# Kernel optimization log

Measured on AMD Instinct MI355X. Metric: run time of the kernel, lower is better.

## Reference

```python
import jax, jax.numpy as jnp
import numpy as np

_EPS = 1e-8
TEMPERATURE = 0.1  # head_cfg.temperature
WEIGHT = 1.0       # float(head_cfg.weight[1:]) with weight='w1'
N = 100000
K = 31   # nsample - 1
C = 64
NUM_CLASSES = 17


def setup_inputs() -> dict:
    key = jax.random.key(0)
    k1, k2, k3 = jax.random.split(key, 3)
    features = jax.random.normal(k1, (N, C), dtype=jnp.float32)
    labels = jax.random.randint(k2, (N,), 0, NUM_CLASSES, dtype=jnp.int32)
    # KNN neighbor indices with self excluded (original drops idx[...,1:]);
    # offset trick guarantees neighbor_idx[i, j] != i.
    off = jax.random.randint(k3, (N, K), 1, N, dtype=jnp.int32)
    neighbor_idx = (jnp.arange(N, dtype=jnp.int32)[:, None] + off) % N
    return {"features": features, "labels": labels, "neighbor_idx": neighbor_idx}


def reference(features, labels, neighbor_idx):
    # posmask_cnt: argmax of one-hot labels == integer class-id comparison
    neighbor_label = labels[neighbor_idx]                      # (N, K) int
    posmask = labels[:, None] == neighbor_label                # (N, K) bool
    cnt = posmask.sum(axis=1)
    point_mask = (cnt > 0) & (cnt < K)                          # (N,) bool

    # dist_l2 on gathered neighbor features
    neighbor_feature = features[neighbor_idx]                  # (N, K, C)
    diff = features[:, None, :] - neighbor_feature             # (N, K, C)
    dist = jnp.sqrt(jnp.sum(diff * diff, axis=-1)) + _EPS      # (N, K)

    # contrast_softnn
    logits = -dist
    logits = logits - jnp.max(logits, axis=1, keepdims=True)
    logits = logits / TEMPERATURE
    exp = jnp.exp(logits)                                      # (N, K)
    pos = jnp.sum(exp * posmask, axis=1)
    neg = jnp.sum(exp, axis=1)
    loss = -jnp.log(pos / neg + _EPS)                          # (N,)

    # masked mean == torch.mean(loss[point_mask])
    pm = point_mask.astype(loss.dtype)
    denom = jnp.maximum(jnp.sum(pm), 1.0)
    return jnp.sum(loss * pm) / denom * WEIGHT
```

## Files before the change

kernel.cpp:

```cpp
#include <hip/hip_runtime.h>
#include <hip/hip_fp16.h>

#define KNB 31
#define CH 64
#define TEMP_INV 10.0f

typedef _Float16 h2 __attribute__((ext_vector_type(2)));
typedef float f2 __attribute__((ext_vector_type(2)));


__global__ void ch_init_ws(double* __restrict__ ws, unsigned* __restrict__ ctr) {
    ws[0] = 0.0;
    ws[1] = 0.0;
    *ctr  = 0u;
}

__global__ __launch_bounds__(256) void ch_cvt8(
    const float* __restrict__ in, unsigned char* __restrict__ out,
    double* __restrict__ ws, unsigned* __restrict__ ctr, int total8)
{
    const int idx = blockIdx.x * blockDim.x + threadIdx.x;
    if (idx == 0) { ws[0] = 0.0; ws[1] = 0.0; *ctr = 0u; }
    if (idx >= total8) return;
    const float4* ip = reinterpret_cast<const float4*>(in) + (size_t)idx * 2;
    const float4 a = ip[0];
    const float4 b = ip[1];
    unsigned lo = 0u, hi = 0u;
    lo = __builtin_amdgcn_cvt_pk_fp8_f32(a.x, a.y, lo, false);
    lo = __builtin_amdgcn_cvt_pk_fp8_f32(a.z, a.w, lo, true);
    hi = __builtin_amdgcn_cvt_pk_fp8_f32(b.x, b.y, hi, false);
    hi = __builtin_amdgcn_cvt_pk_fp8_f32(b.z, b.w, hi, true);
    uint2 o; o.x = lo; o.y = hi;
    reinterpret_cast<uint2*>(out)[idx] = o;
}

__device__ __forceinline__ void fp8_to_f32x16(const uint4 u, float* f) {
    union { uint4 v; unsigned w[4]; } U;
    U.v = u;
    #pragma unroll
    for (int q = 0; q < 4; ++q) {
        const f2 p0 = __builtin_amdgcn_cvt_pk_f32_fp8(U.w[q], false);
        const f2 p1 = __builtin_amdgcn_cvt_pk_f32_fp8(U.w[q], true);
        f[4 * q + 0] = p0[0]; f[4 * q + 1] = p0[1];
        f[4 * q + 2] = p1[0]; f[4 * q + 3] = p1[1];
    }
}

__device__ __forceinline__ float fp8_sub_sq_acc(const float* fA, const uint4 bu, float s) {
    union { uint4 v; unsigned w[4]; } U;
    U.v = bu;
    #pragma unroll
    for (int q = 0; q < 4; ++q) {
        const f2 p0 = __builtin_amdgcn_cvt_pk_f32_fp8(U.w[q], false);
        const f2 p1 = __builtin_amdgcn_cvt_pk_f32_fp8(U.w[q], true);
        float d;
        d = fA[4 * q + 0] - p0[0]; s = fmaf(d, d, s);
        d = fA[4 * q + 1] - p0[1]; s = fmaf(d, d, s);
        d = fA[4 * q + 2] - p1[0]; s = fmaf(d, d, s);
        d = fA[4 * q + 3] - p1[1]; s = fmaf(d, d, s);
    }
    return s;
}

__global__ __launch_bounds__(256)
__attribute__((amdgpu_waves_per_eu(2, 4)))
void ch_main8q2(
    const unsigned char* __restrict__ tab8,
    const int*           __restrict__ labels,
    const int*           __restrict__ nidx,
    double*              __restrict__ ws,
    unsigned*            __restrict__ ctr,
    float*               __restrict__ out,
    int n)
{
    const int t    = threadIdx.x;
    const int qid  = t >> 2;
    const int sub  = t & 3;
    const int i0   = blockIdx.x * 128 + qid;
    const int i1   = i0 + 64;
    const bool v0  = (i0 < n);
    const bool v1  = (i1 < n);
    const int i0c  = v0 ? i0 : 0;
    const int i1c  = v1 ? i1 : 0;

    float loss_w = 0.0f;
    float pm_f   = 0.0f;

    if (v0) {
        float fA0[16], fA1[16];
        fp8_to_f32x16(reinterpret_cast<const uint4*>(tab8 + (size_t)i0c * CH)[sub], fA0);
        fp8_to_f32x16(reinterpret_cast<const uint4*>(tab8 + (size_t)i1c * CH)[sub], fA1);

        const int lab0 = labels[i0c];
        const int lab1 = labels[i1c];
        const int* nrow0 = nidx + (size_t)i0c * KNB;
        const int* nrow1 = nidx + (size_t)i1c * KNB;

        float m0 = -1e30f, se0 = 0.0f, sp0 = 0.0f;
        float m1 = -1e30f, se1 = 0.0f, sp1 = 0.0f;
        int cnt0 = 0, cnt1 = 0;

        #pragma unroll 2
        for (int j = 0; j < KNB; ++j) {
            const int nj0 = nrow0[j];
            const int nj1 = nrow1[j];

            const uint4 b0 = reinterpret_cast<const uint4*>(tab8 + (size_t)nj0 * CH)[sub];
            const uint4 b1 = reinterpret_cast<const uint4*>(tab8 + (size_t)nj1 * CH)[sub];

            float s0 = fp8_sub_sq_acc(fA0, b0, 0.0f);
            float s1 = fp8_sub_sq_acc(fA1, b1, 0.0f);

            s0 += __shfl_xor(s0, 1);
            s0 += __shfl_xor(s0, 2);
            s1 += __shfl_xor(s1, 1);
            s1 += __shfl_xor(s1, 2);

            const float l0 = -(sqrtf(s0) + 1e-8f);
            const float l1 = -(sqrtf(s1) + 1e-8f);

            const bool pm0 = (labels[nj0] == lab0);
            const bool pm1 = (labels[nj1] == lab1);
            cnt0 += pm0 ? 1 : 0;
            cnt1 += pm1 ? 1 : 0;

            if (l0 > m0) {
                const float r = __expf((m0 - l0) * TEMP_INV);
                se0 *= r; sp0 *= r; m0 = l0;
            }
            const float e0 = __expf((l0 - m0) * TEMP_INV);
            se0 += e0;
            if (pm0) sp0 += e0;

            if (l1 > m1) {
                const float r = __expf((m1 - l1) * TEMP_INV);
                se1 *= r; sp1 *= r; m1 = l1;
            }
            const float e1 = __expf((l1 - m1) * TEMP_INV);
            se1 += e1;
            if (pm1) sp1 += e1;
        }

        if (sub == 0) {
            if (v0 && cnt0 > 0 && cnt0 < KNB) {
                loss_w += -logf(sp0 / se0 + 1e-8f);
                pm_f   += 1.0f;
            }
            if (v1 && cnt1 > 0 && cnt1 < KNB) {
                loss_w += -logf(sp1 / se1 + 1e-8f);
                pm_f   += 1.0f;
            }
        }
    }

    __shared__ float s_l[256];
    __shared__ float s_c[256];
    s_l[t] = loss_w;
    s_c[t] = pm_f;
    __syncthreads();
    #pragma unroll
    for (int off = 128; off > 0; off >>= 1) {
        if (t < off) {
            s_l[t] += s_l[t + off];
            s_c[t] += s_c[t + off];
        }
        __syncthreads();
    }
    if (t == 0) {
        atomicAdd(ws,     (double)s_l[0]);
        atomicAdd(ws + 1, (double)s_c[0]);
        __threadfence();
        const unsigned old = atomicAdd(ctr, 1u);
        if (old == gridDim.x - 1) {
            const double sl = atomicAdd(ws, 0.0);
            const double sc = atomicAdd(ws + 1, 0.0);
            const double c  = (sc < 1.0) ? 1.0 : sc;
            out[0] = (float)(sl / c);
        }
    }
}

__global__ __launch_bounds__(256) void ch_cvt(
    const float* __restrict__ in, __half* __restrict__ out, int total8)
{
    const int idx = blockIdx.x * blockDim.x + threadIdx.x;
    if (idx >= total8) return;
    const float4* ip = reinterpret_cast<const float4*>(in) + (size_t)idx * 2;
    const float4 a = ip[0];
    const float4 b = ip[1];
    union { uint4 u; __half2 h[4]; } o;
    o.h[0] = __floats2half2_rn(a.x, a.y);
    o.h[1] = __floats2half2_rn(a.z, a.w);
    o.h[2] = __floats2half2_rn(b.x, b.y);
    o.h[3] = __floats2half2_rn(b.z, b.w);
    reinterpret_cast<uint4*>(out)[idx] = o.u;
}

__device__ __forceinline__ float dot2acc(h2 d, float s) {
    return __builtin_amdgcn_fdot2(d, d, s, false);
}

template <bool FP16>
__global__ __launch_bounds__(256) void ch_main4(
    const float*  __restrict__ feat,
    const __half* __restrict__ tab,
    const int*    __restrict__ labels,
    const int*    __restrict__ nidx,
    double*       __restrict__ ws,
    int n)
{
    const int t   = threadIdx.x;
    const int i   = blockIdx.x * (256 / 4) + (t >> 2);
    const int sub = t & 3;

    float loss_w = 0.0f;
    float pm_f   = 0.0f;

    if (i < n) {
        float f[16];
        union { uint4 u[2]; h2 h[8]; } A;
        if constexpr (FP16) {
            const uint4* ap = reinterpret_cast<const uint4*>(tab + (size_t)i * CH + sub * 16);
            A.u[0] = ap[0];
            A.u[1] = ap[1];
        } else {
            const float4* ap = reinterpret_cast<const float4*>(feat + (size_t)i * CH + sub * 16);
            #pragma unroll
            for (int q = 0; q < 4; ++q) {
                const float4 v = ap[q];
                f[4 * q]     = v.x;
                f[4 * q + 1] = v.y;
                f[4 * q + 2] = v.z;
                f[4 * q + 3] = v.w;
            }
        }

        const int lab = labels[i];
        float m = -1e30f, se = 0.0f, sp = 0.0f;
        int cnt = 0;

        #pragma unroll 2
        for (int j = 0; j < KNB; ++j) {
            const int nj = nidx[(size_t)i * KNB + j];

            float s = 0.0f;
            if constexpr (FP16) {
                union { uint4 u[2]; h2 h[8]; } B;
                const uint4* bp = reinterpret_cast<const uint4*>(tab + (size_t)nj * CH + sub * 16);
                B.u[0] = bp[0];
                B.u[1] = bp[1];
                #pragma unroll
                for (int q = 0; q < 8; ++q) {
                    const h2 d = A.h[q] - B.h[q];
                    s = dot2acc(d, s);
                }
            } else {
                const float4* bp = reinterpret_cast<const float4*>(feat + (size_t)nj * CH + sub * 16);
                #pragma unroll
                for (int q = 0; q < 4; ++q) {
                    const float4 v = bp[q];
                    const float dx = f[4 * q]     - v.x;
                    const float dy = f[4 * q + 1] - v.y;
                    const float dz = f[4 * q + 2] - v.z;
                    const float dw = f[4 * q + 3] - v.w;
                    s += dx * dx + dy * dy + dz * dz + dw * dw;
                }
            }
            s += __shfl_xor(s, 1);
            s += __shfl_xor(s, 2);

            const float l = -(sqrtf(s) + 1e-8f);
            const bool pm = (labels[nj] == lab);
            cnt += pm ? 1 : 0;

            if (l > m) {
                const float r = __expf((m - l) * TEMP_INV);
                se *= r; sp *= r; m = l;
            }
            const float e = __expf((l - m) * TEMP_INV);
            se += e;
            if (pm) sp += e;
        }

        if (sub == 0 && cnt > 0 && cnt < KNB) {
            loss_w = -logf(sp / se + 1e-8f);
            pm_f   = 1.0f;
        }
    }

    __shared__ float s_l[256];
    __shared__ float s_c[256];
    s_l[t] = loss_w;
    s_c[t] = pm_f;
    __syncthreads();
    #pragma unroll
    for (int off = 128; off > 0; off >>= 1) {
        if (t < off) {
            s_l[t] += s_l[t + off];
            s_c[t] += s_c[t + off];
        }
        __syncthreads();
    }
    if (t == 0) {
        atomicAdd(ws,     (double)s_l[0]);
        atomicAdd(ws + 1, (double)s_c[0]);
    }
}

__global__ void ch_finalize(const double* __restrict__ ws, float* __restrict__ out) {
    double c = ws[1];
    if (c < 1.0) c = 1.0;
    out[0] = (float)(ws[0] / c);
}

extern "C" void kernel_launch(void* const* d_in, const int* in_sizes, int n_in,
                              void* d_out, int out_size, void* d_ws, size_t ws_size,
                              hipStream_t stream) {
    const float* feat   = (const float*)d_in[0];
    const int*   labels = (const int*)d_in[1];
    const int*   nidx   = (const int*)d_in[2];
    float*       out    = (float*)d_out;
    double*      ws     = (double*)d_ws;
    unsigned*    ctr    = (unsigned*)((char*)d_ws + 16);

    const int n = in_sizes[1];
    const int total8 = n * CH / 8;

    if (ws_size >= 256 + (size_t)n * CH) {
        unsigned char* tab = (unsigned char*)d_ws + 256;
        ch_cvt8<<<(total8 + 255) / 256, 256, 0, stream>>>(feat, tab, ws, ctr, total8);
        const int blocks = (n + 127) / 128;
        ch_main8q2<<<blocks, 256, 0, stream>>>(tab, labels, nidx, ws, ctr, out, n);
        return;
    }

    ch_init_ws<<<1, 1, 0, stream>>>(ws, ctr);
    const int blocks = (n + 63) / 64;
    if (ws_size >= 256 + (size_t)n * CH * 2) {
        __half* tab = reinterpret_cast<__half*>((char*)d_ws + 256);
        ch_cvt<<<(total8 + 255) / 256, 256, 0, stream>>>(feat, tab, total8);
        ch_main4<true><<<blocks, 256, 0, stream>>>(feat, tab, labels, nidx, ws, n);
    } else {
        ch_main4<false><<<blocks, 256, 0, stream>>>(feat, nullptr, labels, nidx, ws, n);
    }
    ch_finalize<<<1, 1, 0, stream>>>(ws, out);
}
```

Baseline: 83.32 us.

## Split each point's neighbor loop into two interleaved online-softmax streams

Each group of four lanes now handles one point instead of two. The 31 neighbors are processed as two interleaved chains of 16 and 15, each keeping its own max and sums, and the chains are merged at the end. The positive count becomes a bitmask with popcount. This doubles the block count and halves the registers holding the query features, aiming for more occupancy while keeping two independent gather streams in flight. The waves_per_eu hint is removed and each thread now does less total work, which adds a merge step and some predication overhead.

```diff
diff --git a/kernel.cpp b/kernel.cpp
--- a/kernel.cpp
+++ b/kernel.cpp
@@ -62,9 +62,7 @@
     return s;
 }
 
-__global__ __launch_bounds__(256)
-__attribute__((amdgpu_waves_per_eu(2, 4)))
-void ch_main8q2(
+__global__ __launch_bounds__(256) void ch_main8d(
     const unsigned char* __restrict__ tab8,
     const int*           __restrict__ labels,
     const int*           __restrict__ nidx,
@@ -73,43 +71,35 @@
     float*               __restrict__ out,
     int n)
 {
-    const int t    = threadIdx.x;
-    const int qid  = t >> 2;
-    const int sub  = t & 3;
-    const int i0   = blockIdx.x * 128 + qid;
-    const int i1   = i0 + 64;
-    const bool v0  = (i0 < n);
-    const bool v1  = (i1 < n);
-    const int i0c  = v0 ? i0 : 0;
-    const int i1c  = v1 ? i1 : 0;
+    const int t   = threadIdx.x;
+    const int i   = blockIdx.x * (256 / 4) + (t >> 2);
+    const int sub = t & 3;
 
     float loss_w = 0.0f;
     float pm_f   = 0.0f;
 
-    if (v0) {
-        float fA0[16], fA1[16];
-        fp8_to_f32x16(reinterpret_cast<const uint4*>(tab8 + (size_t)i0c * CH)[sub], fA0);
-        fp8_to_f32x16(reinterpret_cast<const uint4*>(tab8 + (size_t)i1c * CH)[sub], fA1);
-
-        const int lab0 = labels[i0c];
-        const int lab1 = labels[i1c];
-        const int* nrow0 = nidx + (size_t)i0c * KNB;
-        const int* nrow1 = nidx + (size_t)i1c * KNB;
+    if (i < n) {
+        float fA[16];
+        fp8_to_f32x16(reinterpret_cast<const uint4*>(tab8 + (size_t)i * CH)[sub], fA);
+
+        const int lab   = labels[i];
+        const int* nrow = nidx + (size_t)i * KNB;
 
         float m0 = -1e30f, se0 = 0.0f, sp0 = 0.0f;
         float m1 = -1e30f, se1 = 0.0f, sp1 = 0.0f;
-        int cnt0 = 0, cnt1 = 0;
+        unsigned pmask = 0u;
 
         #pragma unroll 2
-        for (int j = 0; j < KNB; ++j) {
-            const int nj0 = nrow0[j];
-            const int nj1 = nrow1[j];
+        for (int j = 0; j < 16; ++j) {
+            const bool c1  = (j < 15);
+            const int  nj0 = nrow[j];
+            const int  nj1 = nrow[c1 ? (j + 16) : 30];
 
             const uint4 b0 = reinterpret_cast<const uint4*>(tab8 + (size_t)nj0 * CH)[sub];
             const uint4 b1 = reinterpret_cast<const uint4*>(tab8 + (size_t)nj1 * CH)[sub];
 
-            float s0 = fp8_sub_sq_acc(fA0, b0, 0.0f);
-            float s1 = fp8_sub_sq_acc(fA1, b1, 0.0f);
+            float s0 = fp8_sub_sq_acc(fA, b0, 0.0f);
+            float s1 = fp8_sub_sq_acc(fA, b1, 0.0f);
 
             s0 += __shfl_xor(s0, 1);
             s0 += __shfl_xor(s0, 2);
@@ -119,10 +109,8 @@
             const float l0 = -(sqrtf(s0) + 1e-8f);
             const float l1 = -(sqrtf(s1) + 1e-8f);
 
-            const bool pm0 = (labels[nj0] == lab0);
-            const bool pm1 = (labels[nj1] == lab1);
-            cnt0 += pm0 ? 1 : 0;
-            cnt1 += pm1 ? 1 : 0;
+            const bool pm0 = (labels[nj0] == lab);
+            pmask |= pm0 ? (1u << j) : 0u;
 
             if (l0 > m0) {
                 const float r = __expf((m0 - l0) * TEMP_INV);
@@ -132,24 +120,30 @@
             se0 += e0;
             if (pm0) sp0 += e0;
 
-            if (l1 > m1) {
-                const float r = __expf((m1 - l1) * TEMP_INV);
-                se1 *= r; sp1 *= r; m1 = l1;
-            }
-            const float e1 = __expf((l1 - m1) * TEMP_INV);
-            se1 += e1;
-            if (pm1) sp1 += e1;
-        }
-
-        if (sub == 0) {
-            if (v0 && cnt0 > 0 && cnt0 < KNB) {
-                loss_w += -logf(sp0 / se0 + 1e-8f);
-                pm_f   += 1.0f;
-            }
-            if (v1 && cnt1 > 0 && cnt1 < KNB) {
-                loss_w += -logf(sp1 / se1 + 1e-8f);
-                pm_f   += 1.0f;
-            }
+            if (c1) {
+                const bool pm1 = (labels[nj1] == lab);
+                pmask |= pm1 ? (1u << (j + 16)) : 0u;
+
+                if (l1 > m1) {
+                    const float r = __expf((m1 - l1) * TEMP_INV);
+                    se1 *= r; sp1 *= r; m1 = l1;
+                }
+                const float e1 = __expf((l1 - m1) * TEMP_INV);
+                se1 += e1;
+                if (pm1) sp1 += e1;
+            }
+        }
+
+        const float mm = fmaxf(m0, m1);
+        const float r0 = __expf((m0 - mm) * TEMP_INV);
+        const float r1 = __expf((m1 - mm) * TEMP_INV);
+        const float se = se0 * r0 + se1 * r1;
+        const float sp = sp0 * r0 + sp1 * r1;
+
+        const int cnt = __popc(pmask);
+        if (sub == 0 && cnt > 0 && cnt < KNB) {
+            loss_w = -logf(sp / se + 1e-8f);
+            pm_f   = 1.0f;
         }
     }
 
@@ -329,8 +323,8 @@
     if (ws_size >= 256 + (size_t)n * CH) {
         unsigned char* tab = (unsigned char*)d_ws + 256;
         ch_cvt8<<<(total8 + 255) / 256, 256, 0, stream>>>(feat, tab, ws, ctr, total8);
-        const int blocks = (n + 127) / 128;
-        ch_main8q2<<<blocks, 256, 0, stream>>>(tab, labels, nidx, ws, ctr, out, n);
+        const int blocks = (n + 63) / 64;
+        ch_main8d<<<blocks, 256, 0, stream>>>(tab, labels, nidx, ws, ctr, out, n);
         return;
     }
 
```

Result: slower. 111.9 us (+34.3%).
